# Optimization experiments

Measured on AMD Instinct MI355X. Metric: run time of the kernel, lower is better.

The kernel has to match this reference:

```python
import jax, jax.numpy as jnp
import numpy as np

B, N, K, D = 2, 32768, 16, 64
EPS = 1e-6

def setup_inputs() -> dict:
    key = jax.random.key(0)
    k1, k2, k3, k4, k5, k6 = jax.random.split(key, 6)
    coords = jax.random.normal(k1, (B, N, 3), dtype=jnp.float32)
    features = jax.random.normal(k2, (B, D, N, 1), dtype=jnp.float32)
    idx = jax.random.randint(k3, (B, N, K), 0, N, dtype=jnp.int32)
    dist = jax.random.uniform(k4, (B, N, K), dtype=jnp.float32)
    conv_w = jax.random.normal(k5, (D, 10), dtype=jnp.float32) * 0.3  # 1x1 conv weight
    conv_b = jax.random.normal(k6, (D,), dtype=jnp.float32) * 0.01
    bn_gamma = jnp.ones((D,), dtype=jnp.float32)
    bn_beta = jnp.zeros((D,), dtype=jnp.float32)
    return {"coords": coords, "features": features, "dist": dist,
            "conv_w": conv_w, "conv_b": conv_b,
            "bn_gamma": bn_gamma, "bn_beta": bn_beta, "idx": idx}

def reference(coords, features, dist, conv_w, conv_b, bn_gamma, bn_beta, idx):
    # gather neighbor coords: (B, N, K, 3)
    neighbors = jax.vmap(lambda c, i: c[i])(coords, idx)
    center = jnp.broadcast_to(coords[:, :, None, :], (B, N, K, 3))
    # relative-position encoding: center | neighbor | center-neighbor | dist -> 10 channels
    concat = jnp.concatenate([center, neighbors, center - neighbors, dist[..., None]], axis=-1)
    # 1x1 conv == channel matmul: (B,N,K,10) @ (D,10)^T -> (B,N,K,D)
    x = jnp.einsum('bnkc,dc->bnkd', concat, conv_w) + conv_b
    # BatchNorm2d in training mode: batch stats over (B,N,K) per channel, eps=1e-6
    mean = jnp.mean(x, axis=(0, 1, 2))
    var = jnp.var(x, axis=(0, 1, 2))
    x = (x - mean) * jax.lax.rsqrt(var + EPS) * bn_gamma + bn_beta
    x = jax.nn.relu(x)
    x = jnp.transpose(x, (0, 3, 1, 2))  # (B, D, N, K)
    feat = jnp.broadcast_to(features, (B, D, N, K))
    return jnp.concatenate([x, feat], axis=1)  # (B, 2D, N, K)
```

## Files before the change

### kernel.cpp

```cpp
#include <hip/hip_runtime.h>

#define BB 2
#define NN 32768
#define KK 16
#define DD 64
#define NC 10
#define NMOM 65
#define NBLK1 256
#define BN_EPS 1e-6

__host__ __device__ __forceinline__ constexpr int pair_idx(int i, int j) {
    return 10 + i * 10 - (i * (i - 1)) / 2 + (j - i);
}

__global__ __launch_bounds__(256) void k_moments(
    const float* __restrict__ coords, const float* __restrict__ dist,
    const int* __restrict__ idx, float* __restrict__ partials)
{
    const int tid = threadIdx.x;
    const int bn = blockIdx.x * 256 + tid;
    const int b = bn >> 15;

    float acc[NMOM];
#pragma unroll
    for (int v = 0; v < NMOM; ++v) acc[v] = 0.f;

    const float cx = coords[(size_t)bn * 3 + 0];
    const float cy = coords[(size_t)bn * 3 + 1];
    const float cz = coords[(size_t)bn * 3 + 2];
    const float* cb = coords + (size_t)b * NN * 3;

    for (int k = 0; k < KK; ++k) {
        const int j = idx[(size_t)bn * KK + k];
        const float nx = cb[(size_t)j * 3 + 0];
        const float ny = cb[(size_t)j * 3 + 1];
        const float nz = cb[(size_t)j * 3 + 2];
        const float dd = dist[(size_t)bn * KK + k];
        const float c[NC] = {cx, cy, cz, nx, ny, nz, cx - nx, cy - ny, cz - nz, dd};
#pragma unroll
        for (int i = 0; i < NC; ++i) acc[i] += c[i];
#pragma unroll
        for (int i = 0; i < NC; ++i)
#pragma unroll
            for (int jj = i; jj < NC; ++jj)
                acc[pair_idx(i, jj)] += c[i] * c[jj];
    }

    __shared__ float red[4 * NMOM];
    const int lane = tid & 63, wave = tid >> 6;
#pragma unroll
    for (int v = 0; v < NMOM; ++v) {
        float x = acc[v];
        x += __shfl_down(x, 32);
        x += __shfl_down(x, 16);
        x += __shfl_down(x, 8);
        x += __shfl_down(x, 4);
        x += __shfl_down(x, 2);
        x += __shfl_down(x, 1);
        if (lane == 0) red[wave * NMOM + v] = x;
    }
    __syncthreads();
    if (tid < NMOM) {
        float p = red[tid] + red[NMOM + tid] + red[2 * NMOM + tid] + red[3 * NMOM + tid];
        partials[blockIdx.x * NMOM + tid] = p;
    }
}

__global__ __launch_bounds__(256) void k_finalize(
    const float* __restrict__ partials,
    const float* __restrict__ conv_w, const float* __restrict__ conv_b,
    const float* __restrict__ gamma, const float* __restrict__ beta,
    float* __restrict__ wscaled, float* __restrict__ bias2)
{
    __shared__ double sums[NMOM];
    const int tid = threadIdx.x;
    if (tid < NMOM) {
        double s = 0.0;
        for (int blk = 0; blk < NBLK1; ++blk)
            s += (double)partials[blk * NMOM + tid];
        sums[tid] = s;
    }
    __syncthreads();
    if (tid < DD) {
        const double cnt = (double)BB * NN * KK;
        double m[NC], w[NC];
#pragma unroll
        for (int c = 0; c < NC; ++c) {
            m[c] = sums[c] / cnt;
            w[c] = (double)conv_w[tid * NC + c];
        }
        const double bd = (double)conv_b[tid];
        double wm = 0.0;
#pragma unroll
        for (int c = 0; c < NC; ++c) wm += w[c] * m[c];
        const double mean = wm + bd;
        double ex2 = bd * bd + 2.0 * bd * wm;
#pragma unroll
        for (int i = 0; i < NC; ++i)
#pragma unroll
            for (int j = i; j < NC; ++j) {
                const double Mij = sums[pair_idx(i, j)] / cnt;
                ex2 += (i == j ? 1.0 : 2.0) * w[i] * w[j] * Mij;
            }
        const double var = ex2 - mean * mean;
        const double scale = (double)gamma[tid] / sqrt(var + BN_EPS);
        bias2[tid] = (float)((double)beta[tid] + (bd - mean) * scale);
#pragma unroll
        for (int c = 0; c < NC; ++c)
            wscaled[tid * NC + c] = (float)(w[c] * scale);
    }
}

__global__ __launch_bounds__(256) void k_main(
    const float* __restrict__ coords, const float* __restrict__ features,
    const float* __restrict__ dist, const int* __restrict__ idx,
    const float* __restrict__ wscaled, const float* __restrict__ bias2,
    float* __restrict__ out)
{
    __shared__ float w_s[DD * NC];
    __shared__ float b2_s[DD];
    const int tid = threadIdx.x;
    for (int i = tid; i < DD * NC; i += 256) w_s[i] = wscaled[i];
    if (tid < DD) b2_s[tid] = bias2[tid];
    __syncthreads();

    const int t = blockIdx.x * 256 + tid;
    const int bn = t >> 2;
    const int b = bn >> 15;
    const int n = bn & (NN - 1);
    const int k0 = (t & 3) << 2;

    const float* cc = coords + (size_t)bn * 3;
    const float cx = cc[0], cy = cc[1], cz = cc[2];
    const float* cb = coords + (size_t)b * NN * 3;

    const int4 j4 = *reinterpret_cast<const int4*>(idx + (size_t)bn * KK + k0);
    const float4 d4 = *reinterpret_cast<const float4*>(dist + (size_t)bn * KK + k0);
    const int js[4] = {j4.x, j4.y, j4.z, j4.w};
    const float dsv[4] = {d4.x, d4.y, d4.z, d4.w};

    float c[4][NC];
#pragma unroll
    for (int q = 0; q < 4; ++q) {
        const float* nc = cb + (size_t)js[q] * 3;
        const float nx = nc[0], ny = nc[1], nz = nc[2];
        c[q][0] = cx; c[q][1] = cy; c[q][2] = cz;
        c[q][3] = nx; c[q][4] = ny; c[q][5] = nz;
        c[q][6] = cx - nx; c[q][7] = cy - ny; c[q][8] = cz - nz;
        c[q][9] = dsv[q];
    }

    const size_t cstride = (size_t)NN * KK;
    const size_t base = (size_t)b * (2 * DD) * cstride + (size_t)n * KK + k0;
    const float* fbase = features + (size_t)b * DD * NN + n;

#pragma unroll 4
    for (int d = 0; d < DD; ++d) {
        const float b2 = b2_s[d];
        float r0 = b2, r1 = b2, r2 = b2, r3 = b2;
#pragma unroll
        for (int cc2 = 0; cc2 < NC; ++cc2) {
            const float w = w_s[d * NC + cc2];
            r0 += c[0][cc2] * w;
            r1 += c[1][cc2] * w;
            r2 += c[2][cc2] * w;
            r3 += c[3][cc2] * w;
        }
        float4 r;
        r.x = fmaxf(r0, 0.f); r.y = fmaxf(r1, 0.f);
        r.z = fmaxf(r2, 0.f); r.w = fmaxf(r3, 0.f);
        *reinterpret_cast<float4*>(out + base + (size_t)d * cstride) = r;

        const float f = fbase[(size_t)d * NN];
        *reinterpret_cast<float4*>(out + base + (size_t)(DD + d) * cstride) =
            float4{f, f, f, f};
    }
}

extern "C" void kernel_launch(void* const* d_in, const int* in_sizes, int n_in,
                              void* d_out, int out_size, void* d_ws, size_t ws_size,
                              hipStream_t stream) {
    const float* coords   = (const float*)d_in[0];
    const float* features = (const float*)d_in[1];
    const float* dist     = (const float*)d_in[2];
    const float* conv_w   = (const float*)d_in[3];
    const float* conv_b   = (const float*)d_in[4];
    const float* gamma    = (const float*)d_in[5];
    const float* beta     = (const float*)d_in[6];
    const int*   idx      = (const int*)d_in[7];
    float* out = (float*)d_out;

    float* partials = (float*)d_ws;
    float* wscaled  = partials + NBLK1 * NMOM;
    float* bias2    = wscaled + DD * NC;

    k_moments<<<NBLK1, 256, 0, stream>>>(coords, dist, idx, partials);
    k_finalize<<<1, 256, 0, stream>>>(partials, conv_w, conv_b, gamma, beta,
                                      wscaled, bias2);
    k_main<<<(BB * NN * KK / 4) / 256, 256, 0, stream>>>(
        coords, features, dist, idx, wscaled, bias2, out);
}
```

Measured before the change: 686.0 us.

## Split feature broadcast into separate kernel and parallelize finalize reduction

Moves the feature-broadcast half of the output into a dedicated kernel where each thread reads one feature value and writes 16 contiguous floats. The main kernel then only computes and writes the conv/BN/ReLU half. Finalize also splits its partial-sum reduction across four thread groups, using 320 threads. This aims to replace the strided feature reads in the main loop with coalesced reads and writes, at the cost of an extra kernel launch.

```diff
diff --git a/kernel.cpp b/kernel.cpp
--- a/kernel.cpp
+++ b/kernel.cpp
@@ -66,33 +66,38 @@
     }
 }
 
-__global__ __launch_bounds__(256) void k_finalize(
+__global__ __launch_bounds__(320) void k_finalize(
     const float* __restrict__ partials,
     const float* __restrict__ conv_w, const float* __restrict__ conv_b,
     const float* __restrict__ gamma, const float* __restrict__ beta,
     float* __restrict__ wscaled, float* __restrict__ bias2)
 {
+    __shared__ double part[4][NMOM];
     __shared__ double sums[NMOM];
     const int tid = threadIdx.x;
-    if (tid < NMOM) {
+    const int g = tid / NMOM, m = tid % NMOM;
+    if (g < 4) {
         double s = 0.0;
-        for (int blk = 0; blk < NBLK1; ++blk)
-            s += (double)partials[blk * NMOM + tid];
-        sums[tid] = s;
-    }
+        for (int blk = g * 64; blk < (g + 1) * 64; ++blk)
+            s += (double)partials[blk * NMOM + m];
+        part[g][m] = s;
+    }
+    __syncthreads();
+    if (tid < NMOM)
+        sums[tid] = part[0][tid] + part[1][tid] + part[2][tid] + part[3][tid];
     __syncthreads();
     if (tid < DD) {
         const double cnt = (double)BB * NN * KK;
-        double m[NC], w[NC];
+        double mm[NC], w[NC];
 #pragma unroll
         for (int c = 0; c < NC; ++c) {
-            m[c] = sums[c] / cnt;
+            mm[c] = sums[c] / cnt;
             w[c] = (double)conv_w[tid * NC + c];
         }
         const double bd = (double)conv_b[tid];
         double wm = 0.0;
 #pragma unroll
-        for (int c = 0; c < NC; ++c) wm += w[c] * m[c];
+        for (int c = 0; c < NC; ++c) wm += w[c] * mm[c];
         const double mean = wm + bd;
         double ex2 = bd * bd + 2.0 * bd * wm;
 #pragma unroll
@@ -111,9 +116,9 @@
     }
 }
 
-__global__ __launch_bounds__(256) void k_main(
-    const float* __restrict__ coords, const float* __restrict__ features,
-    const float* __restrict__ dist, const int* __restrict__ idx,
+__global__ __launch_bounds__(256) void k_x(
+    const float* __restrict__ coords, const float* __restrict__ dist,
+    const int* __restrict__ idx,
     const float* __restrict__ wscaled, const float* __restrict__ bias2,
     float* __restrict__ out)
 {
@@ -152,7 +157,6 @@
 
     const size_t cstride = (size_t)NN * KK;
     const size_t base = (size_t)b * (2 * DD) * cstride + (size_t)n * KK + k0;
-    const float* fbase = features + (size_t)b * DD * NN + n;
 
 #pragma unroll 4
     for (int d = 0; d < DD; ++d) {
@@ -170,11 +174,22 @@
         r.x = fmaxf(r0, 0.f); r.y = fmaxf(r1, 0.f);
         r.z = fmaxf(r2, 0.f); r.w = fmaxf(r3, 0.f);
         *reinterpret_cast<float4*>(out + base + (size_t)d * cstride) = r;
-
-        const float f = fbase[(size_t)d * NN];
-        *reinterpret_cast<float4*>(out + base + (size_t)(DD + d) * cstride) =
-            float4{f, f, f, f};
-    }
+    }
+}
+
+__global__ __launch_bounds__(256) void k_feat(
+    const float* __restrict__ features, float* __restrict__ out)
+{
+    const int t = blockIdx.x * 256 + threadIdx.x;
+    const float f = features[t];
+    const int bd = t >> 15;
+    const int n = t & (NN - 1);
+    const int b = bd >> 6;
+    const int d = bd & (DD - 1);
+    const size_t base = (((size_t)b * 2 * DD + DD + d) * NN + n) * KK;
+    const float4 v{f, f, f, f};
+    float4* p = reinterpret_cast<float4*>(out + base);
+    p[0] = v; p[1] = v; p[2] = v; p[3] = v;
 }
 
 extern "C" void kernel_launch(void* const* d_in, const int* in_sizes, int n_in,
@@ -195,8 +210,9 @@
     float* bias2    = wscaled + DD * NC;
 
     k_moments<<<NBLK1, 256, 0, stream>>>(coords, dist, idx, partials);
-    k_finalize<<<1, 256, 0, stream>>>(partials, conv_w, conv_b, gamma, beta,
+    k_finalize<<<1, 320, 0, stream>>>(partials, conv_w, conv_b, gamma, beta,
                                       wscaled, bias2);
-    k_main<<<(BB * NN * KK / 4) / 256, 256, 0, stream>>>(
-        coords, features, dist, idx, wscaled, bias2, out);
-}
+    k_feat<<<(BB * DD * NN) / 256, 256, 0, stream>>>(features, out);
+    k_x<<<(BB * NN * KK / 4) / 256, 256, 0, stream>>>(
+        coords, dist, idx, wscaled, bias2, out);
+}
```

Measured after the change: 652.5 us. 4.9% less time.
